# Kernel tuning notes

Hardware: AMD Instinct MI355X
Metric: run time of the kernel (lower is better)

## Reference

```python
import jax, jax.numpy as jnp
import numpy as np

VOCAB, D, H, L, SEQ = 32000, 768, 12, 6, 1024
HD = D // H
DFF = 4 * D
EPS = 1e-5


def _ln(x, g, b):
    mu = jnp.mean(x, axis=-1, keepdims=True)
    var = jnp.var(x, axis=-1, keepdims=True)
    return (x - mu) * jax.lax.rsqrt(var + EPS) * g + b


def setup_inputs() -> dict:
    key = jax.random.key(0)
    ks = jax.random.split(key, 10)
    s = lambda *sh: 0.02
    return {
        "idx": jax.random.randint(ks[0], (2, SEQ), 0, VOCAB, dtype=jnp.int64) if jax.config.jax_enable_x64 else jax.random.randint(ks[0], (2, SEQ), 0, VOCAB, dtype=jnp.int32),
        "tok_emb": jax.random.normal(ks[1], (VOCAB, D), jnp.float32) * 0.02,
        "pos_emb": jax.random.normal(ks[2], (SEQ, D), jnp.float32) * 0.02,
        "Wqkv": jax.random.normal(ks[3], (L, D, 3 * D), jnp.float32) * 0.02,
        "bqkv": jnp.zeros((L, 3 * D), jnp.float32),
        "Wo": jax.random.normal(ks[4], (L, D, D), jnp.float32) * 0.02,
        "bo": jnp.zeros((L, D), jnp.float32),
        "ln1_g": jnp.ones((L, D), jnp.float32),
        "ln1_b": jnp.zeros((L, D), jnp.float32),
        "ln2_g": jnp.ones((L, D), jnp.float32),
        "ln2_b": jnp.zeros((L, D), jnp.float32),
        "W1": jax.random.normal(ks[5], (L, D, DFF), jnp.float32) * 0.02,
        "b1": jnp.zeros((L, DFF), jnp.float32),
        "W2": jax.random.normal(ks[6], (L, DFF, D), jnp.float32) * 0.02,
        "b2": jnp.zeros((L, D), jnp.float32),
        "lnf_g": jnp.ones((D,), jnp.float32),
        "lnf_b": jnp.zeros((D,), jnp.float32),
        "Wlm": jax.random.normal(ks[7], (D, VOCAB), jnp.float32) * 0.02,
    }


def _forward(idx, tok_emb, pos_emb, Wqkv, bqkv, Wo, bo, ln1_g, ln1_b,
             ln2_g, ln2_b, W1, b1, W2, b2, lnf_g, lnf_b, Wlm):
    B, T = idx.shape
    x = tok_emb[idx] + pos_emb[None, :T]  # [B,T,D]
    causal = jnp.tril(jnp.ones((T, T), bool))  # [T,T]
    for l in range(L):
        h = _ln(x, ln1_g[l], ln1_b[l])
        qkv = h @ Wqkv[l] + bqkv[l]  # [B,T,3D]
        qkv = qkv.reshape(B, T, 3, H, HD).transpose(2, 0, 3, 1, 4)
        q, k, v = qkv[0], qkv[1], qkv[2]  # each [B,H,T,HD]
        att = jnp.einsum('bhqd,bhkd->bhqk', q, k) / np.sqrt(HD).astype(np.float32)
        att = jnp.where(causal, att, -jnp.inf)
        att = jax.nn.softmax(att, axis=-1)
        o = jnp.einsum('bhqk,bhkd->bhqd', att, v)
        o = o.transpose(0, 2, 1, 3).reshape(B, T, D)
        x = x + o @ Wo[l] + bo[l]
        h = _ln(x, ln2_g[l], ln2_b[l])
        x = x + jax.nn.gelu(h @ W1[l] + b1[l], approximate=False) @ W2[l] + b2[l]
    x = _ln(x, lnf_g, lnf_b)
    return x @ Wlm  # [B,T,VOCAB]


def reference(idx, tok_emb, pos_emb, Wqkv, bqkv, Wo, bo, ln1_g, ln1_b,
              ln2_g, ln2_b, W1, b1, W2, b2, lnf_g, lnf_b, Wlm):
    return _forward(idx, tok_emb, pos_emb, Wqkv, bqkv, Wo, bo, ln1_g, ln1_b,
                    ln2_g, ln2_b, W1, b1, W2, b2, lnf_g, lnf_b, Wlm)
```

## Files before the change

kernel.cpp:

```cpp
#include <hip/hip_runtime.h>
#include <math.h>

#define TT   1024
#define DD   768
#define HH   12
#define LLAY 6
#define DFFN 3072
#define BB   2
#define NTOK (BB*TT)

typedef __bf16 bf16;
typedef __attribute__((ext_vector_type(8))) __bf16 bf16x8;
typedef __attribute__((ext_vector_type(4))) __bf16 bf16x4;
typedef __attribute__((ext_vector_type(4))) float f32x4;

__device__ inline unsigned pack_bf16x2(float a, float b) {
    union { bf16 h[2]; unsigned u; } un;
    un.h[0] = (bf16)a; un.h[1] = (bf16)b;
    return un.u;
}

__device__ inline void gload16(const bf16* g, bf16* l) {
    __builtin_amdgcn_global_load_lds((const void*)g, (void*)l, 16, 0, 0);
}

template<int N> __device__ inline void waitcnt_vm() {
    if constexpr (N == 0) asm volatile("s_waitcnt vmcnt(0)" ::: "memory");
    else if constexpr (N == 3) asm volatile("s_waitcnt vmcnt(3)" ::: "memory");
    else if constexpr (N == 4) asm volatile("s_waitcnt vmcnt(4)" ::: "memory");
    else if constexpr (N == 8) asm volatile("s_waitcnt vmcnt(8)" ::: "memory");
}

__global__ __launch_bounds__(256) void embed_kernel(const int* __restrict__ idx,
                                                    const float* __restrict__ tok,
                                                    const float* __restrict__ pos,
                                                    float* __restrict__ x) {
    int bt = blockIdx.x;
    int t  = bt % TT;
    int id = idx[bt];
    const float* te = tok + (size_t)id * DD;
    const float* pe = pos + (size_t)t * DD;
    float* xr = x + (size_t)bt * DD;
    for (int d = threadIdx.x; d < DD; d += 256) xr[d] = te[d] + pe[d];
}

__global__ __launch_bounds__(256) void ln_kernel(const float* __restrict__ in,
                                                 const float* __restrict__ g,
                                                 const float* __restrict__ b,
                                                 bf16* __restrict__ out) {
    const int wid = threadIdx.x >> 6, lane = threadIdx.x & 63;
    const int row = blockIdx.x * 4 + wid;
    const float* xr = in + (size_t)row * DD;
    float4 v[3];
    float s = 0.f, s2 = 0.f;
#pragma unroll
    for (int j = 0; j < 3; ++j) {
        v[j] = *(const float4*)&xr[lane * 4 + 256 * j];
        s  += v[j].x + v[j].y + v[j].z + v[j].w;
        s2 += v[j].x * v[j].x + v[j].y * v[j].y + v[j].z * v[j].z + v[j].w * v[j].w;
    }
    for (int off = 32; off; off >>= 1) { s += __shfl_down(s, off); s2 += __shfl_down(s2, off); }
    s = __shfl(s, 0); s2 = __shfl(s2, 0);
    const float mu = s / (float)DD;
    const float rs = rsqrtf(s2 / (float)DD - mu * mu + 1e-5f);
    bf16* orow = out + (size_t)row * DD;
#pragma unroll
    for (int j = 0; j < 3; ++j) {
        float4 gg = *(const float4*)&g[lane * 4 + 256 * j];
        float4 bb = *(const float4*)&b[lane * 4 + 256 * j];
        bf16x4 o;
        o[0] = (bf16)((v[j].x - mu) * rs * gg.x + bb.x);
        o[1] = (bf16)((v[j].y - mu) * rs * gg.y + bb.y);
        o[2] = (bf16)((v[j].z - mu) * rs * gg.z + bb.z);
        o[3] = (bf16)((v[j].w - mu) * rs * gg.w + bb.w);
        *(bf16x4*)&orow[lane * 4 + 256 * j] = o;
    }
}

__device__ inline void convT_tile(const float* __restrict__ in, bf16* __restrict__ out,
                                  int K, int N, int k0, int n0) {
    __shared__ float tile[32][33];
    int tn = threadIdx.x & 31, tk = threadIdx.x >> 5;
#pragma unroll
    for (int i = 0; i < 4; ++i)
        tile[tk + i * 8][tn] = in[(size_t)(k0 + tk + i * 8) * N + n0 + tn];
    __syncthreads();
#pragma unroll
    for (int i = 0; i < 4; ++i)
        out[(size_t)(n0 + tk + i * 8) * K + k0 + tn] = (bf16)tile[tn][tk + i * 8];
}

__global__ __launch_bounds__(256) void convT_kernel(const float* __restrict__ in,
                                                    bf16* __restrict__ out,
                                                    int K, int N) {
    convT_tile(in, out, K, N, blockIdx.y * 32, blockIdx.x * 32);
}

__global__ __launch_bounds__(256) void convT4_kernel(const float* __restrict__ w0,
                                                     const float* __restrict__ w1,
                                                     const float* __restrict__ w2,
                                                     const float* __restrict__ w3,
                                                     bf16* __restrict__ o0,
                                                     bf16* __restrict__ o1,
                                                     bf16* __restrict__ o2,
                                                     bf16* __restrict__ o3) {
    int bid = blockIdx.x;
    const float* in; bf16* out; int K, N, t;
    if (bid < 1728)      { in = w0; out = o0; K = 768;  N = 2304; t = bid; }
    else if (bid < 2304) { in = w1; out = o1; K = 768;  N = 768;  t = bid - 1728; }
    else if (bid < 4608) { in = w2; out = o2; K = 768;  N = 3072; t = bid - 2304; }
    else                 { in = w3; out = o3; K = 3072; N = 768;  t = bid - 4608; }
    int nt = N / 32;
    convT_tile(in, out, K, N, (t / nt) * 32, (t % nt) * 32);
}

template<int BM, int EPI>
__global__ __launch_bounds__(256) void mgemm(const bf16* __restrict__ A,
                                             const bf16* __restrict__ Bt,
                                             const float* __restrict__ bias,
                                             const float* __restrict__ res,
                                             void* __restrict__ Cout,
                                             bf16* __restrict__ vtout,
                                             int M, int N, int K) {
    constexpr int MF = BM / 32;
    constexpr int NF = 4;
    constexpr int AIT = BM / 64;
    constexpr int STG = AIT + 2;
    constexpr int ASZ = BM * 32;
    constexpr int BUFE = ASZ + 128 * 32;
    __shared__ __align__(16) bf16 smem[3 * BUFE];
    int bm = blockIdx.y * BM;
    int bn = blockIdx.x * 128;
    int tid = threadIdx.x;
    int lane = tid & 63;
    int w = tid >> 6;
    int wr = w >> 1, wc = w & 1;
    int l15 = lane & 15, g = lane >> 4;

    f32x4 acc[MF][NF];
#pragma unroll
    for (int m = 0; m < MF; ++m)
#pragma unroll
        for (int n = 0; n < NF; ++n) acc[m][n] = (f32x4){0.f, 0.f, 0.f, 0.f};

    int r = lane >> 2;
    int koff = ((lane & 3) ^ ((r >> 1) & 3)) * 8;
    const bf16* Ab = A + (size_t)(bm + w * 16 + r) * K + koff;
    const bf16* Bb = Bt + (size_t)(bn + w * 16 + r) * K + koff;

    auto stage = [&](int p, int k0) {
        bf16* base = smem + p * BUFE;
        bf16* Asb = base + w * 16 * 32;
        bf16* Bsb = base + ASZ + w * 16 * 32;
#pragma unroll
        for (int it = 0; it < AIT; ++it)
            gload16(Ab + (size_t)(it * 64) * K + k0, Asb + it * 64 * 32);
#pragma unroll
        for (int it = 0; it < 2; ++it)
            gload16(Bb + (size_t)(it * 64) * K + k0, Bsb + it * 64 * 32);
    };

    stage(0, 0);
    stage(1, 32);
    waitcnt_vm<STG>();
    __builtin_amdgcn_s_barrier();
    int cur = 0;

    for (int k0 = 0; k0 < K; k0 += 32) {
        const bf16* Ac = smem + cur * BUFE;
        const bf16* Bc = Ac + ASZ;
        bf16x8 af[MF], bfv[NF];
#pragma unroll
        for (int m = 0; m < MF; ++m) {
            int row = wr * (BM / 2) + m * 16 + l15;
            int gs = g ^ ((row >> 1) & 3);
            af[m] = *(const bf16x8*)&Ac[row * 32 + gs * 8];
        }
#pragma unroll
        for (int n = 0; n < NF; ++n) {
            int row = wc * 64 + n * 16 + l15;
            int gs = g ^ ((row >> 1) & 3);
            bfv[n] = *(const bf16x8*)&Bc[row * 32 + gs * 8];
        }
        bool st = (k0 + 64 < K);
        if (st) {
            int nxt = cur + 2; if (nxt >= 3) nxt -= 3;
            stage(nxt, k0 + 64);
        }
#pragma unroll
        for (int m = 0; m < MF; ++m)
#pragma unroll
            for (int n = 0; n < NF; ++n)
                acc[m][n] = __builtin_amdgcn_mfma_f32_16x16x32_bf16(af[m], bfv[n], acc[m][n], 0, 0, 0);
        if (st) waitcnt_vm<STG>();
        else    waitcnt_vm<0>();
        __builtin_amdgcn_s_barrier();
        cur = (cur == 2) ? 0 : cur + 1;
    }

    int lq = g * 4;
#pragma unroll
    for (int m = 0; m < MF; ++m) {
#pragma unroll
        for (int n = 0; n < NF; ++n) {
            int col = bn + wc * 64 + n * 16 + l15;
            float bv = bias[col];
            if (EPI == 4 && col >= 2 * DD) {
                int row0 = bm + wr * (BM / 2) + m * 16 + lq;
                int b = row0 >> 10, t0 = row0 & 1023;
                int hd = col - 2 * DD;
                union { bf16 h[4]; unsigned long long u; } pk;
#pragma unroll
                for (int j = 0; j < 4; ++j) pk.h[j] = (bf16)(acc[m][n][j] + bv);
                *(unsigned long long*)&vtout[((size_t)(b * DD + hd)) * TT + t0] = pk.u;
            } else {
#pragma unroll
                for (int j = 0; j < 4; ++j) {
                    int row = bm + wr * (BM / 2) + m * 16 + lq + j;
                    float v = acc[m][n][j] + bv;
                    if (EPI == 2) {
                        ((float*)Cout)[(size_t)row * N + col] = v + res[(size_t)row * N + col];
                    } else if (EPI == 3) {
                        v = 0.5f * v * (1.f + erff(v * 0.70710678118654752f));
                        ((bf16*)Cout)[(size_t)row * N + col] = (bf16)v;
                    } else if (EPI == 1) {
                        ((bf16*)Cout)[(size_t)row * N + col] = (bf16)v;
                    } else {
                        if (col < DD) v *= 0.125f;
                        ((bf16*)Cout)[(size_t)row * N + col] = (bf16)v;
                    }
                }
            }
        }
    }
}

__global__ __launch_bounds__(512, 2) void lmgemm(const bf16* __restrict__ A,
                                                 const bf16* __restrict__ Bt,
                                                 float* __restrict__ C) {
    constexpr int ABUF = 256 * 32;
    constexpr int BUFE = 2 * ABUF;
    __shared__ __align__(16) bf16 smem[4 * BUFE];
    const int tid = threadIdx.x;
    const int w = tid >> 6, lane = tid & 63;
    const int wm = w >> 2, wn = w & 3;
    const int l15 = lane & 15, g = lane >> 4;
    const int bm = blockIdx.x * 256;
    const int bn = blockIdx.y * 256;

    const int fcol = ((g ^ ((l15 >> 1) & 3))) * 8;

    const int rA = lane >> 2;
    const int csw = ((lane & 3) ^ ((lane >> 3) & 3)) * 8;
    const bf16* a0 = A  + (size_t)(bm + w * 16 + rA) * DD + csw;
    const bf16* b0 = Bt + (size_t)(bn + w * 16 + rA) * DD + csw;
    const int ld0 = (w * 16) * 32;
    const int ld1 = (w * 16 + 128) * 32;

    f32x4 acc[8][4];
#pragma unroll
    for (int m = 0; m < 8; ++m)
#pragma unroll
        for (int n = 0; n < 4; ++n) acc[m][n] = (f32x4){0.f, 0.f, 0.f, 0.f};

    auto stagef = [&](int p, int kelem) {
        bf16* base = smem + p * BUFE;
        gload16(a0 + kelem, base + ld0);
        gload16(a0 + (size_t)128 * DD + kelem, base + ld1);
        gload16(b0 + kelem, base + ABUF + ld0);
        gload16(b0 + (size_t)128 * DD + kelem, base + ABUF + ld1);
    };

    stagef(0, 0);
    stagef(1, 32);
    stagef(2, 64);
    waitcnt_vm<8>();
    __builtin_amdgcn_s_barrier();

    for (int t = 0; t < 21; ++t) {
        const bf16* Ar = smem + (t & 3) * BUFE;
        const bf16* Br = Ar + ABUF;
        bf16x8 af[8], bfv[4];
#pragma unroll
        for (int m = 0; m < 8; ++m)
            af[m] = *(const bf16x8*)&Ar[(wm * 128 + m * 16 + l15) * 32 + fcol];
#pragma unroll
        for (int n = 0; n < 4; ++n)
            bfv[n] = *(const bf16x8*)&Br[(wn * 64 + n * 16 + l15) * 32 + fcol];
        stagef((t + 3) & 3, (t + 3) * 32);
        __builtin_amdgcn_s_setprio(1);
#pragma unroll
        for (int m = 0; m < 8; ++m)
#pragma unroll
            for (int n = 0; n < 4; ++n)
                acc[m][n] = __builtin_amdgcn_mfma_f32_16x16x32_bf16(af[m], bfv[n], acc[m][n], 0, 0, 0);
        __builtin_amdgcn_s_setprio(0);
        waitcnt_vm<8>();
        __builtin_amdgcn_s_barrier();
    }
    waitcnt_vm<0>();
    __builtin_amdgcn_s_barrier();
#pragma unroll
    for (int t = 21; t < 24; ++t) {
        const bf16* Ar = smem + (t & 3) * BUFE;
        const bf16* Br = Ar + ABUF;
        bf16x8 af[8], bfv[4];
#pragma unroll
        for (int m = 0; m < 8; ++m)
            af[m] = *(const bf16x8*)&Ar[(wm * 128 + m * 16 + l15) * 32 + fcol];
#pragma unroll
        for (int n = 0; n < 4; ++n)
            bfv[n] = *(const bf16x8*)&Br[(wn * 64 + n * 16 + l15) * 32 + fcol];
#pragma unroll
        for (int m = 0; m < 8; ++m)
#pragma unroll
            for (int n = 0; n < 4; ++n)
                acc[m][n] = __builtin_amdgcn_mfma_f32_16x16x32_bf16(af[m], bfv[n], acc[m][n], 0, 0, 0);
    }

    __syncthreads();
    float* eb = (float*)smem + w * (16 * 68);
    const int rr = lane >> 2, c0 = (lane & 3) * 16;
#pragma unroll
    for (int mf = 0; mf < 8; ++mf) {
#pragma unroll
        for (int n = 0; n < 4; ++n)
#pragma unroll
            for (int j = 0; j < 4; ++j)
                eb[(g * 4 + j) * 68 + n * 16 + l15] = acc[mf][n][j];
        __syncthreads();
        const float* src = &eb[rr * 68 + c0];
        float* dst = C + (size_t)(bm + wm * 128 + mf * 16 + rr) * 32000 + bn + wn * 64 + c0;
        *(float4*)(dst + 0)  = *(const float4*)(src + 0);
        *(float4*)(dst + 4)  = *(const float4*)(src + 4);
        *(float4*)(dst + 8)  = *(const float4*)(src + 8);
        *(float4*)(dst + 12) = *(const float4*)(src + 12);
        __syncthreads();
    }
}

__global__ __launch_bounds__(256) void fattn_kernel(const bf16* __restrict__ qkv,
                                                    const bf16* __restrict__ vt,
                                                    bf16* __restrict__ o) {
    const int bh = blockIdx.y;
    const int b = bh / HH, h = bh % HH;
    const int qc = gridDim.x - 1 - blockIdx.x;
    const int q0 = qc * 64;
    const int tid = threadIdx.x;
    const int w = tid >> 6, lane = tid & 63;
    const int l15 = lane & 15, g = lane >> 4;

    __shared__ __align__(16) bf16 Ks[64 * 64];
    __shared__ __align__(16) bf16 Vs[64 * 64];
    __shared__ __align__(16) bf16 Ps[4][16 * 64];

    const size_t basebt = (size_t)b * TT;
    const int qw = q0 + w * 16;
    const int qg = qw + l15;

    bf16x8 bq0, bq1;
    {
        const bf16* qp = qkv + (basebt + qw + l15) * 2304 + h * 64 + g * 8;
        bq0 = *(const bf16x8*)(qp);
        bq1 = *(const bf16x8*)(qp + 32);
    }

    float mstate = -1e30f, lstate = 0.f;
    f32x4 oacc[4];
#pragma unroll
    for (int nf = 0; nf < 4; ++nf) oacc[nf] = (f32x4){0.f, 0.f, 0.f, 0.f};

    const int swzA = (l15 & 7) << 4;
    char* const psBase = (char*)&Ps[w][0];

    const int nchunk = qc + 1;
    for (int c = 0; c < nchunk; ++c) {
        const int kc = c * 64;
        __syncthreads();
        {
            int r0 = tid >> 3;
            int e0 = (tid & 7) * 8;
#pragma unroll
            for (int i = 0; i < 2; ++i) {
                int r = r0 + 32 * i;
                int swzW = (r & 7) << 4;
                bf16x8 kv = *(const bf16x8*)&qkv[(basebt + kc + r) * 2304 + DD + h * 64 + e0];
                *(bf16x8*)((char*)Ks + r * 128 + ((e0 * 2) ^ swzW)) = kv;
                bf16x8 vv = *(const bf16x8*)&vt[((size_t)bh * 64 + r) * TT + kc + e0];
                *(bf16x8*)((char*)Vs + r * 128 + ((e0 * 2) ^ swzW)) = vv;
            }
        }
        __syncthreads();
        if (kc > qw + 15) continue;

        f32x4 s[4];
        __builtin_amdgcn_s_setprio(1);
#pragma unroll
        for (int mf = 0; mf < 4; ++mf) {
            char* kr = (char*)Ks + (16 * mf + l15) * 128;
            bf16x8 ka0 = *(const bf16x8*)(kr + ((16 * g) ^ swzA));
            bf16x8 ka1 = *(const bf16x8*)(kr + ((64 + 16 * g) ^ swzA));
            f32x4 a = (f32x4){0.f, 0.f, 0.f, 0.f};
            a = __builtin_amdgcn_mfma_f32_16x16x32_bf16(ka0, bq0, a, 0, 0, 0);
            a = __builtin_amdgcn_mfma_f32_16x16x32_bf16(ka1, bq1, a, 0, 0, 0);
            s[mf] = a;
        }
        __builtin_amdgcn_s_setprio(0);
        if (kc + 63 > qw) {
#pragma unroll
            for (int mf = 0; mf < 4; ++mf)
#pragma unroll
                for (int j = 0; j < 4; ++j)
                    if (kc + 16 * mf + 4 * g + j > qg) s[mf][j] = -1e30f;
        }
        float cm = -1e30f;
#pragma unroll
        for (int mf = 0; mf < 4; ++mf)
#pragma unroll
            for (int j = 0; j < 4; ++j) cm = fmaxf(cm, s[mf][j]);
        cm = fmaxf(cm, __shfl_xor(cm, 16));
        cm = fmaxf(cm, __shfl_xor(cm, 32));
        float mnew = fmaxf(mstate, cm);
        float sc = __expf(mstate - mnew);
        mstate = mnew;
        float p[4][4];
        float psum = 0.f;
#pragma unroll
        for (int mf = 0; mf < 4; ++mf)
#pragma unroll
            for (int j = 0; j < 4; ++j) { float pv = __expf(s[mf][j] - mnew); p[mf][j] = pv; psum += pv; }
        psum += __shfl_xor(psum, 16);
        psum += __shfl_xor(psum, 32);
        lstate = lstate * sc + psum;
#pragma unroll
        for (int mf = 0; mf < 4; ++mf) {
            unsigned lo = pack_bf16x2(p[mf][0], p[mf][1]);
            unsigned hi = pack_bf16x2(p[mf][2], p[mf][3]);
            char* dst = psBase + l15 * 128 + ((32 * mf + 8 * g) ^ swzA);
            *(unsigned*)dst = lo;
            *(unsigned*)(dst + 4) = hi;
        }
        float s0 = __shfl(sc, 4 * g + 0), s1 = __shfl(sc, 4 * g + 1);
        float s2 = __shfl(sc, 4 * g + 2), s3 = __shfl(sc, 4 * g + 3);
#pragma unroll
        for (int nf = 0; nf < 4; ++nf) {
            oacc[nf][0] *= s0; oacc[nf][1] *= s1; oacc[nf][2] *= s2; oacc[nf][3] *= s3;
        }
        bf16x8 pa0 = *(const bf16x8*)(psBase + l15 * 128 + ((16 * g) ^ swzA));
        bf16x8 pa1 = *(const bf16x8*)(psBase + l15 * 128 + ((64 + 16 * g) ^ swzA));
        __builtin_amdgcn_s_setprio(1);
#pragma unroll
        for (int nf = 0; nf < 4; ++nf) {
            char* vr = (char*)Vs + (16 * nf + l15) * 128;
            bf16x8 vb0 = *(const bf16x8*)(vr + ((16 * g) ^ swzA));
            bf16x8 vb1 = *(const bf16x8*)(vr + ((64 + 16 * g) ^ swzA));
            oacc[nf] = __builtin_amdgcn_mfma_f32_16x16x32_bf16(pa0, vb0, oacc[nf], 0, 0, 0);
            oacc[nf] = __builtin_amdgcn_mfma_f32_16x16x32_bf16(pa1, vb1, oacc[nf], 0, 0, 0);
        }
        __builtin_amdgcn_s_setprio(0);
    }
    float linv = 1.f / lstate;
    float l0 = __shfl(linv, 4 * g + 0), l1 = __shfl(linv, 4 * g + 1);
    float l2 = __shfl(linv, 4 * g + 2), l3 = __shfl(linv, 4 * g + 3);
    float lj[4] = {l0, l1, l2, l3};
#pragma unroll
    for (int j = 0; j < 4; ++j) {
        bf16* orow = o + (size_t)(basebt + qw + 4 * g + j) * DD + h * 64 + l15;
#pragma unroll
        for (int nf = 0; nf < 4; ++nf)
            orow[16 * nf] = (bf16)(oacc[nf][j] * lj[j]);
    }
}

extern "C" void kernel_launch(void* const* d_in, const int* in_sizes, int n_in,
                              void* d_out, int out_size, void* d_ws, size_t ws_size,
                              hipStream_t stream) {
    (void)in_sizes; (void)n_in; (void)out_size; (void)ws_size;
    const int*   idx  = (const int*)d_in[0];
    const float* tok  = (const float*)d_in[1];
    const float* pos  = (const float*)d_in[2];
    const float* Wqkv = (const float*)d_in[3];
    const float* bqkv = (const float*)d_in[4];
    const float* Wo   = (const float*)d_in[5];
    const float* bo   = (const float*)d_in[6];
    const float* ln1g = (const float*)d_in[7];
    const float* ln1b = (const float*)d_in[8];
    const float* ln2g = (const float*)d_in[9];
    const float* ln2b = (const float*)d_in[10];
    const float* W1   = (const float*)d_in[11];
    const float* b1   = (const float*)d_in[12];
    const float* W2   = (const float*)d_in[13];
    const float* b2   = (const float*)d_in[14];
    const float* lnfg = (const float*)d_in[15];
    const float* lnfb = (const float*)d_in[16];
    const float* Wlm  = (const float*)d_in[17];
    float* out = (float*)d_out;

    char* ws = (char*)d_ws;
    float* x     = (float*)(ws);
    bf16*  abuf0 = (bf16*)(ws + 6291456);
    bf16*  abuf1 = (bf16*)(ws + 9437184);
    bf16*  qkvb  = (bf16*)(ws + 22020096);
    bf16*  vtb   = (bf16*)(ws + 31457280);
    bf16*  wbuf  = (bf16*)(ws + 34603008);

    bf16* wq = wbuf;
    bf16* wo = wbuf + 1769472;
    bf16* w1 = wbuf + 2359296;
    bf16* w2 = wbuf + 4718592;

    embed_kernel<<<NTOK, 256, 0, stream>>>(idx, tok, pos, x);

    for (int l = 0; l < LLAY; ++l) {
        convT4_kernel<<<6912, 256, 0, stream>>>(
            Wqkv + (size_t)l * DD * 3 * DD, Wo + (size_t)l * DD * DD,
            W1 + (size_t)l * DD * DFFN, W2 + (size_t)l * DFFN * DD,
            wq, wo, w1, w2);
        ln_kernel<<<NTOK / 4, 256, 0, stream>>>(x, ln1g + l * DD, ln1b + l * DD, abuf0);
        mgemm<128, 4><<<dim3(3 * DD / 128, NTOK / 128), 256, 0, stream>>>(
            abuf0, wq, bqkv + (size_t)l * 3 * DD, nullptr, qkvb, vtb, NTOK, 3 * DD, DD);
        fattn_kernel<<<dim3(TT / 64, BB * HH), 256, 0, stream>>>(qkvb, vtb, abuf0);
        mgemm<64, 2><<<dim3(DD / 128, NTOK / 64), 256, 0, stream>>>(
            abuf0, wo, bo + (size_t)l * DD, x, x, nullptr, NTOK, DD, DD);
        ln_kernel<<<NTOK / 4, 256, 0, stream>>>(x, ln2g + l * DD, ln2b + l * DD, abuf0);
        mgemm<128, 3><<<dim3(DFFN / 128, NTOK / 128), 256, 0, stream>>>(
            abuf0, w1, b1 + (size_t)l * DFFN, nullptr, abuf1, nullptr, NTOK, DFFN, DD);
        mgemm<64, 2><<<dim3(DD / 128, NTOK / 64), 256, 0, stream>>>(
            abuf1, w2, b2 + (size_t)l * DD, x, x, nullptr, NTOK, DD, DFFN);
    }
    ln_kernel<<<NTOK / 4, 256, 0, stream>>>(x, lnfg, lnfb, abuf0);
    convT_kernel<<<dim3(32000 / 32, DD / 32), 256, 0, stream>>>(Wlm, wbuf, DD, 32000);
    lmgemm<<<dim3(NTOK / 256, 32000 / 256), 512, 0, stream>>>(abuf0, wbuf, out);
}
```

Before: 1.005 ms.

## Interleave LDS fragment loads, global stages and MFMA phases in LM-head GEMM

The LM-head GEMM main loop is split into four sub-phases. Each sub-phase loads only two A fragments from LDS, issues one of the four global-to-LDS copies, and runs eight MFMAs, with barriers and explicit lgkmcnt waits between phases. The aim is to spread LDS and global memory traffic across the MFMA work so the matrix units see fewer stalls, in a ping-pong style schedule. In exchange it adds many workgroup barriers per k-step, which can serialize warps and cost more than the overlap gains.

New measurement: 992.8 us. No clear change (-1.2%).

```diff
diff --git a/kernel.cpp b/kernel.cpp
--- a/kernel.cpp
+++ b/kernel.cpp
@@ -248,7 +248,7 @@
     const int bm = blockIdx.x * 256;
     const int bn = blockIdx.y * 256;
 
-    const int fcol = ((g ^ ((l15 >> 1) & 3))) * 8;
+    const int fcol = (g ^ ((l15 >> 1) & 3)) * 8;
 
     const int rA = lane >> 2;
     const int csw = ((lane & 3) ^ ((lane >> 3) & 3)) * 8;
@@ -277,24 +277,47 @@
     waitcnt_vm<8>();
     __builtin_amdgcn_s_barrier();
 
+#define LDA(m) (*(const bf16x8*)&Ar[(wm * 128 + (m) * 16 + l15) * 32 + fcol])
+#define LDB(n) (*(const bf16x8*)&Br[(wn * 64 + (n) * 16 + l15) * 32 + fcol])
+#define WAIT_LGKM0 do { asm volatile("s_waitcnt lgkmcnt(0)" ::: "memory"); \
+                        __builtin_amdgcn_sched_barrier(0); } while (0)
+#define MFMA8(i, j) do { __builtin_amdgcn_s_setprio(1); \
+    _Pragma("unroll") \
+    for (int n = 0; n < 4; ++n) { \
+        acc[i][n] = __builtin_amdgcn_mfma_f32_16x16x32_bf16(af0, bfv[n], acc[i][n], 0, 0, 0); \
+        acc[j][n] = __builtin_amdgcn_mfma_f32_16x16x32_bf16(af1, bfv[n], acc[j][n], 0, 0, 0); } \
+    __builtin_amdgcn_s_setprio(0); } while (0)
+
     for (int t = 0; t < 21; ++t) {
         const bf16* Ar = smem + (t & 3) * BUFE;
         const bf16* Br = Ar + ABUF;
-        bf16x8 af[8], bfv[4];
-#pragma unroll
-        for (int m = 0; m < 8; ++m)
-            af[m] = *(const bf16x8*)&Ar[(wm * 128 + m * 16 + l15) * 32 + fcol];
-#pragma unroll
-        for (int n = 0; n < 4; ++n)
-            bfv[n] = *(const bf16x8*)&Br[(wn * 64 + n * 16 + l15) * 32 + fcol];
-        stagef((t + 3) & 3, (t + 3) * 32);
-        __builtin_amdgcn_s_setprio(1);
-#pragma unroll
-        for (int m = 0; m < 8; ++m)
-#pragma unroll
-            for (int n = 0; n < 4; ++n)
-                acc[m][n] = __builtin_amdgcn_mfma_f32_16x16x32_bf16(af[m], bfv[n], acc[m][n], 0, 0, 0);
-        __builtin_amdgcn_s_setprio(0);
+        bf16* nb = smem + ((t + 3) & 3) * BUFE;
+        const int kel = (t + 3) * 32;
+        bf16x8 af0, af1, bfv[4];
+        bfv[0] = LDB(0); bfv[1] = LDB(1); bfv[2] = LDB(2); bfv[3] = LDB(3);
+        af0 = LDA(0); af1 = LDA(1);
+        gload16(a0 + kel, nb + ld0);
+        __builtin_amdgcn_s_barrier();
+        WAIT_LGKM0;
+        MFMA8(0, 1);
+        __builtin_amdgcn_s_barrier();
+        af0 = LDA(2); af1 = LDA(3);
+        gload16(a0 + (size_t)128 * DD + kel, nb + ld1);
+        __builtin_amdgcn_s_barrier();
+        WAIT_LGKM0;
+        MFMA8(2, 3);
+        __builtin_amdgcn_s_barrier();
+        af0 = LDA(4); af1 = LDA(5);
+        gload16(b0 + kel, nb + ABUF + ld0);
+        __builtin_amdgcn_s_barrier();
+        WAIT_LGKM0;
+        MFMA8(4, 5);
+        __builtin_amdgcn_s_barrier();
+        af0 = LDA(6); af1 = LDA(7);
+        gload16(b0 + (size_t)128 * DD + kel, nb + ABUF + ld1);
+        __builtin_amdgcn_s_barrier();
+        WAIT_LGKM0;
+        MFMA8(6, 7);
         waitcnt_vm<8>();
         __builtin_amdgcn_s_barrier();
     }
@@ -306,17 +329,19 @@
         const bf16* Br = Ar + ABUF;
         bf16x8 af[8], bfv[4];
 #pragma unroll
-        for (int m = 0; m < 8; ++m)
-            af[m] = *(const bf16x8*)&Ar[(wm * 128 + m * 16 + l15) * 32 + fcol];
-#pragma unroll
-        for (int n = 0; n < 4; ++n)
-            bfv[n] = *(const bf16x8*)&Br[(wn * 64 + n * 16 + l15) * 32 + fcol];
+        for (int m = 0; m < 8; ++m) af[m] = LDA(m);
+#pragma unroll
+        for (int n = 0; n < 4; ++n) bfv[n] = LDB(n);
 #pragma unroll
         for (int m = 0; m < 8; ++m)
 #pragma unroll
             for (int n = 0; n < 4; ++n)
                 acc[m][n] = __builtin_amdgcn_mfma_f32_16x16x32_bf16(af[m], bfv[n], acc[m][n], 0, 0, 0);
     }
+#undef LDA
+#undef LDB
+#undef WAIT_LGKM0
+#undef MFMA8
 
     __syncthreads();
     float* eb = (float*)smem + w * (16 * 68);
```
